# Optimization experiments

Hardware: AMD Instinct MI355X
Metric: run time of the kernel (lower is better)

The kernel has to match this reference:

```python
import jax, jax.numpy as jnp
import numpy as np

T, A = 2048, 64          # n_thread, n_agents
RAWOB, N_TP, N_GP = 120, 5, 2
E = N_TP * N_GP          # number of sub-nets (type x group placeholder)
D = RAWOB + N_TP + 1     # augmented obs dim fed to each Net
H = 128                  # hidden width of each sub-net MLP
N_ACTION = 16


def setup_inputs() -> dict:
    key = jax.random.key(0)
    ks = jax.random.split(key, 12)
    s1 = 1.0 / np.sqrt(D)
    s2 = 1.0 / np.sqrt(H)
    return {
        "obs": jax.random.normal(ks[0], (T, A, RAWOB), dtype=jnp.float32),
        "hete_pick": jax.random.randint(ks[1], (T, A), 0, E),
        "hete_type": jax.random.randint(ks[2], (T, A), 0, N_TP),
        "gp_sel_summary": jax.random.randint(ks[3], (T, N_TP), 0, N_GP),
        # per-expert actor MLP params [E, ...]
        "W1": jax.random.normal(ks[4], (E, D, H), dtype=jnp.float32) * s1,
        "b1": jnp.zeros((E, H), dtype=jnp.float32),
        "W2": jax.random.normal(ks[5], (E, H, N_ACTION), dtype=jnp.float32) * s2,
        "b2": jnp.zeros((E, N_ACTION), dtype=jnp.float32),
        # central critic params
        "Wc1": jax.random.normal(ks[6], (D, H), dtype=jnp.float32) * s1,
        "bc1": jnp.zeros((H,), dtype=jnp.float32),
        "Wc2": jax.random.normal(ks[7], (H, 1), dtype=jnp.float32) * s2,
        "bc2": jnp.zeros((1,), dtype=jnp.float32),
    }


def _augment_obs(obs, hete_type, gp_sel_summary):
    # obs <- cat(obs, hete_type, gp_sel_summary with -1 scattered at own type idx)
    t, a, _ = obs.shape
    n_tp = gp_sel_summary.shape[1]
    gp = jnp.broadcast_to(gp_sel_summary[:, None, :].astype(obs.dtype), (t, a, n_tp))
    oh = jax.nn.one_hot(hete_type, n_tp, dtype=obs.dtype)
    gp_obs = gp * (1.0 - oh) - oh  # scatter -1 at index hete_type
    return jnp.concatenate([obs, hete_type[..., None].astype(obs.dtype), gp_obs], axis=-1)


def reference(obs, hete_pick, hete_type, gp_sel_summary,
              W1, b1, W2, b2, Wc1, bc1, Wc2, bc2):
    t, a, _ = obs.shape
    x = _augment_obs(obs, hete_type, gp_sel_summary)          # [T, A, D]
    xf = x.reshape(t * a, -1)                                  # [N, D]
    pick = hete_pick.reshape(t * a)                            # [N]
    n_exp = W1.shape[0]
    # dispatch: each token routed to exactly one sub-net; dense compute + masked combine
    logits = jnp.zeros((t * a, W2.shape[-1]), dtype=obs.dtype)
    for e in range(n_exp):  # small fixed expert loop
        y = jax.nn.relu(xf @ W1[e] + b1[e]) @ W2[e] + b2[e]    # [N, n_action]
        logits = jnp.where((pick == e)[:, None], y, logits)
    logits = logits.reshape(t, a, -1)
    # central critic on all tokens
    value = (jax.nn.relu(xf @ Wc1 + bc1) @ Wc2 + bc2).reshape(t, a, 1)
    return logits, value
```

## Files before the change

kernel.cpp:

```cpp
#include <hip/hip_runtime.h>
#include <hip/hip_bf16.h>

#define T_DIM   2048
#define A_DIM   64
#define N_TOK   (T_DIM * A_DIM)
#define RAWOB   120
#define N_TP    5
#define E_EXP   10
#define D_DIM   126
#define DP      128
#define H_DIM   128
#define N_ACT   16
#define CAP     14336
#define BTOK    128
#define MAXC    (CAP / BTOK)
#define LOGITS_SZ (N_TOK * N_ACT)
#define HB_STRIDE 136

typedef __bf16 bh8 __attribute__((ext_vector_type(8)));
typedef ushort u16x8 __attribute__((ext_vector_type(8)));
typedef float  f32x4 __attribute__((ext_vector_type(4)));

__device__ __forceinline__ f32x4 mfma16(bh8 a, bh8 b, f32x4 c) {
    return __builtin_amdgcn_mfma_f32_16x16x32_bf16(a, b, c, 0, 0, 0);
}

__device__ __forceinline__ ushort f2bf(float f) {
    unsigned x = __builtin_bit_cast(unsigned, f);
    unsigned r = (x + 0x7fffu + ((x >> 16) & 1u)) >> 16;
    return (ushort)r;
}

#define W1P_N (E_EXP * H_DIM * DP)
#define W2P_N (E_EXP * N_ACT * H_DIM)
#define WC1P_N (DP * DP)
#define PREP_BLOCKS 124

__global__ __launch_bounds__(256) void prep_kernel(
    const float* __restrict__ W1, const float* __restrict__ W2,
    const float* __restrict__ Wc1,
    int* __restrict__ counts, ushort* __restrict__ W1p,
    ushort* __restrict__ W2p, ushort* __restrict__ Wc1p)
{
    int bx = blockIdx.x, tid = threadIdx.x;
    if (bx < 44) {
        __shared__ ushort st[32][130];
        const float* src;
        ushort* dstbase;
        int kt;
        if (bx < 40) {
            int e = bx >> 2;
            kt = bx & 3;
            src = W1 + (e * D_DIM + kt * 32) * H_DIM;
            dstbase = W1p + e * (H_DIM * DP);
        } else {
            kt = bx - 40;
            src = Wc1 + kt * 32 * H_DIM;
            dstbase = Wc1p;
        }
        int dmax = D_DIM - kt * 32;
#pragma unroll
        for (int p = 0; p < 16; ++p) {
            int idx = p * 256 + tid;
            int dd = idx >> 7, n = idx & 127;
            float v = (dd < dmax) ? src[dd * H_DIM + n] : 0.f;
            st[dd][n] = f2bf(v);
        }
        __syncthreads();
#pragma unroll
        for (int p = 0; p < 16; ++p) {
            int idx = p * 256 + tid;
            int dd = idx >> 7, n = idx & 127;
            dstbase[((n >> 4) * 4 + kt) * 512 + ((dd >> 3) * 16 + (n & 15)) * 8 + (dd & 7)]
                = st[dd][n];
        }
    } else {
        int i = (bx - 44) * 256 + tid;
        int j = i & 7;
        int l = (i >> 3) & 63;
        int kt = (i >> 9) & 3;
        int e = i >> 11;
        int lm = l & 15, lq = l >> 4;
        W2p[i] = f2bf(W2[(e * H_DIM + kt * 32 + lq * 8 + j) * N_ACT + lm]);
        if (bx == 44 && tid < 160) counts[tid] = 0;
    }
}

#define BUCKET_BLOCKS 128
__global__ __launch_bounds__(256) void bucket_kernel(
    const int* __restrict__ pick, int* __restrict__ counts, int* __restrict__ order)
{
    __shared__ int lc[E_EXP], lb[E_EXP], lcur[E_EXP];
    int tid = threadIdx.x;
    if (tid < E_EXP) { lc[tid] = 0; lcur[tid] = 0; }
    __syncthreads();
    int base = blockIdx.x * 1024;
    int e4[4];
#pragma unroll
    for (int it = 0; it < 4; ++it) {
        e4[it] = pick[base + it * 256 + tid];
        atomicAdd(&lc[e4[it]], 1);
    }
    __syncthreads();
    if (tid < E_EXP) lb[tid] = atomicAdd(&counts[tid * 16], lc[tid]);
    __syncthreads();
#pragma unroll
    for (int it = 0; it < 4; ++it) {
        int e = e4[it];
        int pos = lb[e] + atomicAdd(&lcur[e], 1);
        if (pos < CAP) order[e * CAP + pos] = base + it * 256 + tid;
    }
}

__global__ __launch_bounds__(256, 2) void moe_kernel(
    const float* __restrict__ obs, const int* __restrict__ hete_type,
    const int* __restrict__ gp_sel,
    const float* __restrict__ b1, const float* __restrict__ b2,
    const float* __restrict__ bc1, const float* __restrict__ bc2,
    const int* __restrict__ counts, const int* __restrict__ order,
    const ushort* __restrict__ W1p, const ushort* __restrict__ W2p,
    const ushort* __restrict__ Wc1p, const float* __restrict__ Wc2,
    float* __restrict__ out)
{
    __shared__ __align__(16) ushort wlds[18432];
    __shared__ __align__(16) ushort hbuf[4][32 * HB_STRIDE];

    const int bx = blockIdx.x;
    const int e = bx % E_EXP;
    const int c = bx / E_EXP;
    const int cnt = counts[e * 16];
    const int start = c * BTOK;
    if (start >= cnt) return;

    const int tid = threadIdx.x;
    const int w = tid >> 6;
    const int base = start + w * 32;
    const int l = tid & 63;
    const int lm = l & 15;
    const int lq = l >> 4;

    {
        const u16x8* s1 = (const u16x8*)(const void*)(W1p + e * (H_DIM * DP));
        u16x8* d1 = (u16x8*)(void*)wlds;
#pragma unroll
        for (int p = 0; p < 8; ++p) d1[p * 256 + tid] = s1[p * 256 + tid];
        ((u16x8*)(void*)(wlds + 16384))[tid] =
            ((const u16x8*)(const void*)(W2p + e * 2048))[tid];
    }

    const int* ord_e = order + e * CAP;

    bh8 a[2][4];
#pragma unroll
    for (int mt = 0; mt < 2; ++mt) {
        const int slot = min(base + mt * 16 + lm, cnt - 1);
        const int tok = ord_e[slot];
        const float* orow = obs + tok * RAWOB;
#pragma unroll
        for (int kt = 0; kt < 3; ++kt) {
            const float* p = orow + kt * 32 + lq * 8;
            float4 u0 = *(const float4*)(const void*)p;
            float4 u1 = *(const float4*)(const void*)(p + 4);
            u16x8 t;
            t[0] = f2bf(u0.x); t[1] = f2bf(u0.y); t[2] = f2bf(u0.z); t[3] = f2bf(u0.w);
            t[4] = f2bf(u1.x); t[5] = f2bf(u1.y); t[6] = f2bf(u1.z); t[7] = f2bf(u1.w);
            a[mt][kt] = __builtin_bit_cast(bh8, t);
        }
        u16x8 t;
        if (lq < 3) {
            const float* p = orow + 96 + lq * 8;
            float4 u0 = *(const float4*)(const void*)p;
            float4 u1 = *(const float4*)(const void*)(p + 4);
            t[0] = f2bf(u0.x); t[1] = f2bf(u0.y); t[2] = f2bf(u0.z); t[3] = f2bf(u0.w);
            t[4] = f2bf(u1.x); t[5] = f2bf(u1.y); t[6] = f2bf(u1.z); t[7] = f2bf(u1.w);
        } else {
            int ht = hete_type[tok];
            int tt = tok >> 6;
            t[0] = f2bf((float)ht);
#pragma unroll
            for (int q = 0; q < N_TP; ++q) {
                float g = (q == ht) ? -1.0f : (float)gp_sel[tt * N_TP + q];
                t[1 + q] = f2bf(g);
            }
            t[6] = 0; t[7] = 0;
        }
        a[mt][3] = __builtin_bit_cast(bh8, t);
    }

    float bnv[8], cnv[8], wcv[8];
#pragma unroll
    for (int nt = 0; nt < 8; ++nt) {
        int n = nt * 16 + lm;
        bnv[nt] = b1[e * H_DIM + n];
        cnv[nt] = bc1[n];
        wcv[nt] = Wc2[n];
    }
    const float bb  = b2[e * N_ACT + lm];
    const float bcv = bc2[0];

    __syncthreads();

    ushort* hrow = &hbuf[w][0];
#pragma unroll
    for (int nt = 0; nt < 8; ++nt) {
        const int n = nt * 16 + lm;
        f32x4 ae0 = (f32x4){0.f,0.f,0.f,0.f}, ae1 = ae0;
#pragma unroll
        for (int kt = 0; kt < 4; ++kt) {
            bh8 be = *(const bh8*)(const void*)(wlds + (nt * 4 + kt) * 512 + l * 8);
            ae0 = mfma16(a[0][kt], be, ae0);
            ae1 = mfma16(a[1][kt], be, ae1);
        }
        float bn = bnv[nt];
#pragma unroll
        for (int r = 0; r < 4; ++r) {
            hrow[(lq * 4 + r) * HB_STRIDE + n] = f2bf(fmaxf(ae0[r] + bn, 0.f));
            hrow[(16 + lq * 4 + r) * HB_STRIDE + n] = f2bf(fmaxf(ae1[r] + bn, 0.f));
        }
    }

    {
        f32x4 y0 = (f32x4){0.f,0.f,0.f,0.f}, y1 = y0;
#pragma unroll
        for (int kt = 0; kt < 4; ++kt) {
            bh8 bf = *(const bh8*)(const void*)(wlds + 16384 + kt * 512 + l * 8);
            bh8 h0 = *(const bh8*)(const void*)(hrow + lm * HB_STRIDE + kt * 32 + lq * 8);
            bh8 h1 = *(const bh8*)(const void*)(hrow + (16 + lm) * HB_STRIDE + kt * 32 + lq * 8);
            y0 = mfma16(h0, bf, y0);
            y1 = mfma16(h1, bf, y1);
        }
#pragma unroll
        for (int r = 0; r < 4; ++r) {
            int m0 = lq * 4 + r;
            if (base + m0 < cnt)
                out[ord_e[base + m0] * N_ACT + lm] = y0[r] + bb;
            int m1 = 16 + lq * 4 + r;
            if (base + m1 < cnt)
                out[ord_e[base + m1] * N_ACT + lm] = y1[r] + bb;
        }
    }

    __syncthreads();

    {
        const u16x8* s1 = (const u16x8*)(const void*)Wc1p;
        u16x8* d1 = (u16x8*)(void*)wlds;
#pragma unroll
        for (int p = 0; p < 8; ++p) d1[p * 256 + tid] = s1[p * 256 + tid];
    }
    __syncthreads();

    {
        float part[2][4] = {{0.f,0.f,0.f,0.f},{0.f,0.f,0.f,0.f}};
#pragma unroll
        for (int nt = 0; nt < 8; ++nt) {
            f32x4 ac0 = (f32x4){0.f,0.f,0.f,0.f}, ac1 = ac0;
#pragma unroll
            for (int kt = 0; kt < 4; ++kt) {
                bh8 bc = *(const bh8*)(const void*)(wlds + (nt * 4 + kt) * 512 + l * 8);
                ac0 = mfma16(a[0][kt], bc, ac0);
                ac1 = mfma16(a[1][kt], bc, ac1);
            }
            float cn = cnv[nt], wc = wcv[nt];
#pragma unroll
            for (int r = 0; r < 4; ++r) {
                part[0][r] += fmaxf(ac0[r] + cn, 0.f) * wc;
                part[1][r] += fmaxf(ac1[r] + cn, 0.f) * wc;
            }
        }
#pragma unroll
        for (int mask = 1; mask < 16; mask <<= 1)
#pragma unroll
            for (int mt = 0; mt < 2; ++mt)
#pragma unroll
                for (int r = 0; r < 4; ++r)
                    part[mt][r] += __shfl_xor(part[mt][r], mask, 64);
        if (lm == 0) {
#pragma unroll
            for (int mt = 0; mt < 2; ++mt)
#pragma unroll
                for (int r = 0; r < 4; ++r) {
                    int m = mt * 16 + lq * 4 + r;
                    if (base + m < cnt)
                        out[LOGITS_SZ + ord_e[base + m]] = part[mt][r] + bcv;
                }
        }
    }
}

extern "C" void kernel_launch(void* const* d_in, const int* in_sizes, int n_in,
                              void* d_out, int out_size, void* d_ws, size_t ws_size,
                              hipStream_t stream) {
    const float* obs  = (const float*)d_in[0];
    const int*   pick = (const int*)d_in[1];
    const int*   htyp = (const int*)d_in[2];
    const int*   gp   = (const int*)d_in[3];
    const float* W1   = (const float*)d_in[4];
    const float* b1   = (const float*)d_in[5];
    const float* W2   = (const float*)d_in[6];
    const float* b2   = (const float*)d_in[7];
    const float* Wc1  = (const float*)d_in[8];
    const float* bc1  = (const float*)d_in[9];
    const float* Wc2  = (const float*)d_in[10];
    const float* bc2  = (const float*)d_in[11];
    float* out = (float*)d_out;

    int*    counts = (int*)d_ws;
    int*    order  = counts + 160;
    ushort* W1p    = (ushort*)(order + E_EXP * CAP);
    ushort* W2p    = W1p + W1P_N;
    ushort* Wc1p   = W2p + W2P_N;

    prep_kernel<<<PREP_BLOCKS, 256, 0, stream>>>(
        W1, W2, Wc1, counts, W1p, W2p, Wc1p);
    bucket_kernel<<<BUCKET_BLOCKS, 256, 0, stream>>>(pick, counts, order);
    moe_kernel<<<E_EXP * MAXC, 256, 0, stream>>>(
        obs, htyp, gp, b1, b2, bc1, bc2, counts, order,
        W1p, W2p, Wc1p, Wc2, out);
}
```

Measured before the change: 148.1 us.

## Fuse prep and bucket kernels, use 512-thread MoE blocks with per-tile hidden buffer

Merges the weight-packing and token-bucketing kernels into one launch and zeroes the counts with a memset, removing one kernel launch and its dependency gap. The MoE kernel now uses 512-thread blocks covering 256 tokens, so each block's expert weights loaded into LDS are reused across twice as many tokens. Each wave processes its two 16-row tiles one after another through a smaller hidden buffer, and critic bias and weights are loaded inside the loop instead of held in registers, lowering register and LDS pressure to target 4 blocks per CU. The risks are fewer, larger blocks with more tail imbalance across experts, and the fused prep/bucket launch running packing and bucketing blocks together with no ordering between them.

Result: faster. 140.3 us (-5.3%).

```diff
diff --git a/kernel.cpp b/kernel.cpp
--- a/kernel.cpp
+++ b/kernel.cpp
@@ -12,7 +12,7 @@
 #define H_DIM   128
 #define N_ACT   16
 #define CAP     14336
-#define BTOK    128
+#define BTOK    256
 #define MAXC    (CAP / BTOK)
 #define LOGITS_SZ (N_TOK * N_ACT)
 #define HB_STRIDE 136
@@ -34,13 +34,14 @@
 #define W1P_N (E_EXP * H_DIM * DP)
 #define W2P_N (E_EXP * N_ACT * H_DIM)
 #define WC1P_N (DP * DP)
-#define PREP_BLOCKS 124
-
-__global__ __launch_bounds__(256) void prep_kernel(
+
+#define PB_BLOCKS 252
+
+__global__ __launch_bounds__(256) void prep_bucket_kernel(
     const float* __restrict__ W1, const float* __restrict__ W2,
-    const float* __restrict__ Wc1,
-    int* __restrict__ counts, ushort* __restrict__ W1p,
-    ushort* __restrict__ W2p, ushort* __restrict__ Wc1p)
+    const float* __restrict__ Wc1, const int* __restrict__ pick,
+    int* __restrict__ counts, int* __restrict__ order,
+    ushort* __restrict__ W1p, ushort* __restrict__ W2p, ushort* __restrict__ Wc1p)
 {
     int bx = blockIdx.x, tid = threadIdx.x;
     if (bx < 44) {
@@ -74,7 +75,7 @@
             dstbase[((n >> 4) * 4 + kt) * 512 + ((dd >> 3) * 16 + (n & 15)) * 8 + (dd & 7)]
                 = st[dd][n];
         }
-    } else {
+    } else if (bx < 124) {
         int i = (bx - 44) * 256 + tid;
         int j = i & 7;
         int l = (i >> 3) & 63;
@@ -82,37 +83,30 @@
         int e = i >> 11;
         int lm = l & 15, lq = l >> 4;
         W2p[i] = f2bf(W2[(e * H_DIM + kt * 32 + lq * 8 + j) * N_ACT + lm]);
-        if (bx == 44 && tid < 160) counts[tid] = 0;
-    }
-}
-
-#define BUCKET_BLOCKS 128
-__global__ __launch_bounds__(256) void bucket_kernel(
-    const int* __restrict__ pick, int* __restrict__ counts, int* __restrict__ order)
-{
-    __shared__ int lc[E_EXP], lb[E_EXP], lcur[E_EXP];
-    int tid = threadIdx.x;
-    if (tid < E_EXP) { lc[tid] = 0; lcur[tid] = 0; }
-    __syncthreads();
-    int base = blockIdx.x * 1024;
-    int e4[4];
-#pragma unroll
-    for (int it = 0; it < 4; ++it) {
-        e4[it] = pick[base + it * 256 + tid];
-        atomicAdd(&lc[e4[it]], 1);
-    }
-    __syncthreads();
-    if (tid < E_EXP) lb[tid] = atomicAdd(&counts[tid * 16], lc[tid]);
-    __syncthreads();
-#pragma unroll
-    for (int it = 0; it < 4; ++it) {
-        int e = e4[it];
-        int pos = lb[e] + atomicAdd(&lcur[e], 1);
-        if (pos < CAP) order[e * CAP + pos] = base + it * 256 + tid;
-    }
-}
-
-__global__ __launch_bounds__(256, 2) void moe_kernel(
+    } else {
+        __shared__ int lc[E_EXP], lb[E_EXP], lcur[E_EXP];
+        if (tid < E_EXP) { lc[tid] = 0; lcur[tid] = 0; }
+        __syncthreads();
+        int base = (bx - 124) * 1024;
+        int e4[4];
+#pragma unroll
+        for (int it = 0; it < 4; ++it) {
+            e4[it] = pick[base + it * 256 + tid];
+            atomicAdd(&lc[e4[it]], 1);
+        }
+        __syncthreads();
+        if (tid < E_EXP) lb[tid] = atomicAdd(&counts[tid * 16], lc[tid]);
+        __syncthreads();
+#pragma unroll
+        for (int it = 0; it < 4; ++it) {
+            int e = e4[it];
+            int pos = lb[e] + atomicAdd(&lcur[e], 1);
+            if (pos < CAP) order[e * CAP + pos] = base + it * 256 + tid;
+        }
+    }
+}
+
+__global__ __launch_bounds__(512, 4) void moe_kernel(
     const float* __restrict__ obs, const int* __restrict__ hete_type,
     const int* __restrict__ gp_sel,
     const float* __restrict__ b1, const float* __restrict__ b2,
@@ -123,7 +117,7 @@
     float* __restrict__ out)
 {
     __shared__ __align__(16) ushort wlds[18432];
-    __shared__ __align__(16) ushort hbuf[4][32 * HB_STRIDE];
+    __shared__ __align__(16) ushort hbuf[8][16 * HB_STRIDE];
 
     const int bx = blockIdx.x;
     const int e = bx % E_EXP;
@@ -143,9 +137,10 @@
         const u16x8* s1 = (const u16x8*)(const void*)(W1p + e * (H_DIM * DP));
         u16x8* d1 = (u16x8*)(void*)wlds;
 #pragma unroll
-        for (int p = 0; p < 8; ++p) d1[p * 256 + tid] = s1[p * 256 + tid];
-        ((u16x8*)(void*)(wlds + 16384))[tid] =
-            ((const u16x8*)(const void*)(W2p + e * 2048))[tid];
+        for (int p = 0; p < 4; ++p) d1[p * 512 + tid] = s1[p * 512 + tid];
+        if (tid < 256)
+            ((u16x8*)(void*)(wlds + 16384))[tid] =
+                ((const u16x8*)(const void*)(W2p + e * 2048))[tid];
     }
 
     const int* ord_e = order + e * CAP;
@@ -187,14 +182,9 @@
         a[mt][3] = __builtin_bit_cast(bh8, t);
     }
 
-    float bnv[8], cnv[8], wcv[8];
-#pragma unroll
-    for (int nt = 0; nt < 8; ++nt) {
-        int n = nt * 16 + lm;
-        bnv[nt] = b1[e * H_DIM + n];
-        cnv[nt] = bc1[n];
-        wcv[nt] = Wc2[n];
-    }
+    float bnv[8];
+#pragma unroll
+    for (int nt = 0; nt < 8; ++nt) bnv[nt] = b1[e * H_DIM + nt * 16 + lm];
     const float bb  = b2[e * N_ACT + lm];
     const float bcv = bc2[0];
 
@@ -202,41 +192,33 @@
 
     ushort* hrow = &hbuf[w][0];
 #pragma unroll
-    for (int nt = 0; nt < 8; ++nt) {
-        const int n = nt * 16 + lm;
-        f32x4 ae0 = (f32x4){0.f,0.f,0.f,0.f}, ae1 = ae0;
-#pragma unroll
-        for (int kt = 0; kt < 4; ++kt) {
-            bh8 be = *(const bh8*)(const void*)(wlds + (nt * 4 + kt) * 512 + l * 8);
-            ae0 = mfma16(a[0][kt], be, ae0);
-            ae1 = mfma16(a[1][kt], be, ae1);
-        }
-        float bn = bnv[nt];
-#pragma unroll
-        for (int r = 0; r < 4; ++r) {
-            hrow[(lq * 4 + r) * HB_STRIDE + n] = f2bf(fmaxf(ae0[r] + bn, 0.f));
-            hrow[(16 + lq * 4 + r) * HB_STRIDE + n] = f2bf(fmaxf(ae1[r] + bn, 0.f));
-        }
-    }
-
-    {
-        f32x4 y0 = (f32x4){0.f,0.f,0.f,0.f}, y1 = y0;
+    for (int mt = 0; mt < 2; ++mt) {
+#pragma unroll
+        for (int nt = 0; nt < 8; ++nt) {
+            const int n = nt * 16 + lm;
+            f32x4 ae = (f32x4){0.f, 0.f, 0.f, 0.f};
+#pragma unroll
+            for (int kt = 0; kt < 4; ++kt) {
+                bh8 be = *(const bh8*)(const void*)(wlds + (nt * 4 + kt) * 512 + l * 8);
+                ae = mfma16(a[mt][kt], be, ae);
+            }
+            float bn = bnv[nt];
+#pragma unroll
+            for (int r = 0; r < 4; ++r)
+                hrow[(lq * 4 + r) * HB_STRIDE + n] = f2bf(fmaxf(ae[r] + bn, 0.f));
+        }
+        f32x4 y = (f32x4){0.f, 0.f, 0.f, 0.f};
 #pragma unroll
         for (int kt = 0; kt < 4; ++kt) {
             bh8 bf = *(const bh8*)(const void*)(wlds + 16384 + kt * 512 + l * 8);
-            bh8 h0 = *(const bh8*)(const void*)(hrow + lm * HB_STRIDE + kt * 32 + lq * 8);
-            bh8 h1 = *(const bh8*)(const void*)(hrow + (16 + lm) * HB_STRIDE + kt * 32 + lq * 8);
-            y0 = mfma16(h0, bf, y0);
-            y1 = mfma16(h1, bf, y1);
+            bh8 hf = *(const bh8*)(const void*)(hrow + lm * HB_STRIDE + kt * 32 + lq * 8);
+            y = mfma16(hf, bf, y);
         }
 #pragma unroll
         for (int r = 0; r < 4; ++r) {
-            int m0 = lq * 4 + r;
-            if (base + m0 < cnt)
-                out[ord_e[base + m0] * N_ACT + lm] = y0[r] + bb;
-            int m1 = 16 + lq * 4 + r;
-            if (base + m1 < cnt)
-                out[ord_e[base + m1] * N_ACT + lm] = y1[r] + bb;
+            int m = mt * 16 + lq * 4 + r;
+            if (base + m < cnt)
+                out[ord_e[base + m] * N_ACT + lm] = y[r] + bb;
         }
     }
 
@@ -246,7 +228,7 @@
         const u16x8* s1 = (const u16x8*)(const void*)Wc1p;
         u16x8* d1 = (u16x8*)(void*)wlds;
 #pragma unroll
-        for (int p = 0; p < 8; ++p) d1[p * 256 + tid] = s1[p * 256 + tid];
+        for (int p = 0; p < 4; ++p) d1[p * 512 + tid] = s1[p * 512 + tid];
     }
     __syncthreads();
 
@@ -254,6 +236,7 @@
         float part[2][4] = {{0.f,0.f,0.f,0.f},{0.f,0.f,0.f,0.f}};
 #pragma unroll
         for (int nt = 0; nt < 8; ++nt) {
+            const int n = nt * 16 + lm;
             f32x4 ac0 = (f32x4){0.f,0.f,0.f,0.f}, ac1 = ac0;
 #pragma unroll
             for (int kt = 0; kt < 4; ++kt) {
@@ -261,7 +244,7 @@
                 ac0 = mfma16(a[0][kt], bc, ac0);
                 ac1 = mfma16(a[1][kt], bc, ac1);
             }
-            float cn = cnv[nt], wc = wcv[nt];
+            float cn = bc1[n], wc = Wc2[n];
 #pragma unroll
             for (int r = 0; r < 4; ++r) {
                 part[0][r] += fmaxf(ac0[r] + cn, 0.f) * wc;
@@ -311,10 +294,10 @@
     ushort* W2p    = W1p + W1P_N;
     ushort* Wc1p   = W2p + W2P_N;
 
-    prep_kernel<<<PREP_BLOCKS, 256, 0, stream>>>(
-        W1, W2, Wc1, counts, W1p, W2p, Wc1p);
-    bucket_kernel<<<BUCKET_BLOCKS, 256, 0, stream>>>(pick, counts, order);
-    moe_kernel<<<E_EXP * MAXC, 256, 0, stream>>>(
+    hipMemsetAsync(counts, 0, 160 * sizeof(int), stream);
+    prep_bucket_kernel<<<PB_BLOCKS, 256, 0, stream>>>(
+        W1, W2, Wc1, pick, counts, order, W1p, W2p, Wc1p);
+    moe_kernel<<<E_EXP * MAXC, 512, 0, stream>>>(
         obs, htyp, gp, b1, b2, bc1, bc2, counts, order,
         W1p, W2p, Wc1p, Wc2, out);
 }
```
